# Kernel tuning notes

Measured on AMD Instinct MI355X. Metric: run time of the kernel, lower is better.

The kernel has to match this reference:

```python
import jax, jax.numpy as jnp
import numpy as np

SIZE = 1024      # codebook entries
CODE_DIM = 256   # embedding dim


def setup_inputs() -> dict:
    key = jax.random.key(0)
    k_z, k_w = jax.random.split(key)
    z = jax.random.normal(k_z, (8, CODE_DIM, 16, 32, 32), dtype=jnp.float32)
    # init.uniform_(weight, -1/size, 1/size)
    codebook = jax.random.uniform(
        k_w, (SIZE, CODE_DIM), dtype=jnp.float32,
        minval=-1.0 / SIZE, maxval=1.0 / SIZE)
    return {"z": z, "codebook": codebook}


def reference(z, codebook):
    bs, d, t, h, w = z.shape
    # tokens: [N, d] with N = bs*t*h*w (matches permute(0,2,3,4,1).reshape(-1,d))
    zf = jnp.transpose(z, (0, 2, 3, 4, 1)).reshape(-1, d)
    # squared-distance expansion instead of materializing [size, N, d]:
    # ||z - e||^2 = ||z||^2 - 2 z.e + ||e||^2 ; argmin identical to argmin of norm
    d2 = (jnp.sum(zf * zf, axis=1, keepdims=True)
          - 2.0 * (zf @ codebook.T)
          + jnp.sum(codebook * codebook, axis=1))  # [N, size]
    encoding_indices = jnp.argmin(d2, axis=-1).reshape(bs, t, h, w)
    # gather + permute back to [bs, d, t, h, w]
    quantized = jnp.transpose(codebook[encoding_indices], (0, 4, 1, 2, 3))
    st = z + jax.lax.stop_gradient(quantized - z)  # straight-through output
    return (quantized, st, encoding_indices)
```

## Files before the change

kernel.cpp:

```cpp
#include <hip/hip_runtime.h>
#include <stdint.h>


constexpr int Dd  = 256;
constexpr int SPB = 16384;
constexpr int Nn  = 131072;
constexpr int Kk  = 1024;
constexpr int CCAP = 16;
#define WWIN 2.2e-3f

typedef short short8 __attribute__((ext_vector_type(8)));
typedef float v4f    __attribute__((ext_vector_type(4)));

__device__ __forceinline__ unsigned bf16pk(float a, float b){
  unsigned ua = __float_as_uint(a), ub = __float_as_uint(b);
  ua = (ua + 0x7fffu + ((ua >> 16) & 1u)) >> 16;
  ub = (ub + 0x7fffu + ((ub >> 16) & 1u)) & 0xffff0000u;
  return ua | ub;
}
__device__ __forceinline__ short8 frg(uint4 u){
  union { uint4 a; short8 b; } x; x.a = u; return x.b;
}
__device__ __forceinline__ v4f mfma16(short8 a, short8 b, v4f c){
  return __builtin_amdgcn_mfma_f32_16x16x32_bf16(a, b, c, 0, 0, 0);
}
__device__ __forceinline__ void dma16(const void* g, void* l){
  __builtin_amdgcn_global_load_lds((const __attribute__((address_space(1))) void*)g,
                                   (__attribute__((address_space(3))) void*)l, 16, 0, 0);
}

__global__ __launch_bounds__(64) void cnorm_k(const float* __restrict__ cb,
                                              float* __restrict__ cn){
  const int k = blockIdx.x, l = threadIdx.x;
  const float* row = cb + (size_t)k * Dd;
  float s = 0.f;
  #pragma unroll
  for (int c = 0; c < Dd; c += 64){ float v = row[c + l]; s += v * v; }
  #pragma unroll
  for (int off = 32; off > 0; off >>= 1) s += __shfl_down(s, off, 64);
  if (l == 0) cn[k] = s;
}

__global__ __launch_bounds__(256) void cconv_k(const float* __restrict__ cb,
                                               uint4* __restrict__ Bg){
  const int cc = blockIdx.x, n = threadIdx.x;
  const float* row = cb + (size_t)(cc * 256 + n) * Dd;
  for (int dc = 0; dc < 8; dc++){
    float v[32];
    const float4* rp = (const float4*)(row + dc * 32);
    #pragma unroll
    for (int q = 0; q < 8; q++){
      float4 f = rp[q]; v[4*q]=f.x; v[4*q+1]=f.y; v[4*q+2]=f.z; v[4*q+3]=f.w;
    }
    unsigned hv[16];
    #pragma unroll
    for (int p = 0; p < 16; p++) hv[p] = bf16pk(v[2*p], v[2*p+1]);
    size_t base = ((size_t)cc * 8 + dc) * 1024;
    #pragma unroll
    for (int kq = 0; kq < 4; kq++)
      Bg[base + (size_t)kq*256 + n] = make_uint4(hv[4*kq],hv[4*kq+1],hv[4*kq+2],hv[4*kq+3]);
  }
}

__global__ __launch_bounds__(512, 4) void vq_sweep_k(const float* __restrict__ z,
                                                     const uint4* __restrict__ Bg,
                                                     const float* __restrict__ cnG,
                                                     int* __restrict__ cntW,
                                                     unsigned short* __restrict__ candW,
                                                     int* __restrict__ abestW,
                                                     int* __restrict__ hCntB,
                                                     int* __restrict__ heavyRegion,
                                                     int* __restrict__ idsW,
                                                     float* __restrict__ out){
  __shared__ uint4 Bs[2][2048];
  __shared__ float cnS[1024];
  __shared__ int hN;
  __shared__ int hT[128];

  const int tid = threadIdx.x, bId = blockIdx.x;
  const int w = tid >> 6, ln = tid & 63;
  const int li = ln & 15, lq = ln >> 4;

  if (tid == 0) hN = 0;

  if (w < 4) dma16((const uint4*)cnG + w*64 + ln, (uint4*)&cnS[w*256]);
  int bOff[4];
  #pragma unroll
  for (int j = 0; j < 4; j++){
    const int f = j*512 + tid;
    bOff[j] = (f >> 8)*1024 + ((f >> 6) & 3)*256 + (f & 63);
  }
  #pragma unroll
  for (int j = 0; j < 4; j++)
    dma16(Bg + bOff[j], &Bs[0][j*512 + w*64]);

  const int tok0 = bId * 128;
  const int b = tok0 >> 14;
  const int s0 = tok0 & 16383;
  const float* zb = z + (size_t)b * Dd * SPB + s0;
  short8 aF[8];
  const int tl = w*16 + li;
  #pragma unroll
  for (int kk = 0; kk < 8; kk++){
    float v[8];
    #pragma unroll
    for (int j = 0; j < 8; j++)
      v[j] = zb[(size_t)(kk*32 + lq*8 + j) * SPB + tl];
    union { unsigned u[4]; short8 s8; } x;
    #pragma unroll
    for (int p = 0; p < 4; p++) x.u[p] = bf16pk(v[2*p], v[2*p+1]);
    aF[kk] = x.s8;
  }

  unsigned bestR[4], thrU[4]; int cntR[4];
  #pragma unroll
  for (int i = 0; i < 4; i++){ bestR[i] = 0xFFFFFFFFu; thrU[i] = 0u; cntR[i] = 0; }

  for (int c = 0; c < 16; c++){
    if (c < 15){
      const int cn1 = c + 1;
      const int srcB = (cn1 >> 2)*8192 + (cn1 & 3)*64;
      uint4* dstB = &Bs[cn1 & 1][0];
      #pragma unroll
      for (int j = 0; j < 4; j++)
        dma16(Bg + srcB + bOff[j], dstB + j*512 + w*64);
      asm volatile("s_waitcnt vmcnt(4)" ::: "memory");
    } else {
      asm volatile("s_waitcnt vmcnt(0)" ::: "memory");
    }
    __builtin_amdgcn_s_barrier();
    asm volatile("" ::: "memory");

    v4f acc[4];
    const v4f vz = {0.f, 0.f, 0.f, 0.f};
    #pragma unroll
    for (int ni = 0; ni < 4; ni++) acc[ni] = vz;

    const uint4* Bbase = &Bs[c & 1][lq*64 + li];
    __builtin_amdgcn_s_setprio(1);
    #pragma unroll
    for (int kk = 0; kk < 8; kk++){
      short8 b0 = frg(Bbase[kk*256 +  0]);
      short8 b1 = frg(Bbase[kk*256 + 16]);
      short8 b2 = frg(Bbase[kk*256 + 32]);
      short8 b3 = frg(Bbase[kk*256 + 48]);
      acc[0] = mfma16(aF[kk], b0, acc[0]);
      acc[1] = mfma16(aF[kk], b1, acc[1]);
      acc[2] = mfma16(aF[kk], b2, acc[2]);
      acc[3] = mfma16(aF[kk], b3, acc[3]);
    }
    __builtin_amdgcn_s_setprio(0);

    float cnv[4];
    #pragma unroll
    for (int ni = 0; ni < 4; ni++) cnv[ni] = cnS[c*64 + ni*16 + li];

    const int codeB = c*64 + li;
    #pragma unroll
    for (int r = 0; r < 4; r++){
      unsigned pv[4];
      unsigned pm = 0xFFFFFFFFu;
      #pragma unroll
      for (int ni = 0; ni < 4; ni++){
        float s = fmaf(acc[ni][r], -2.0f, cnv[ni]);
        unsigned u = __float_as_uint(s);
        u ^= (unsigned)((int)u >> 31) | 0x80000000u;
        unsigned p = (u & 0xFFFFFC00u) | (unsigned)(codeB + ni*16);
        pv[ni] = p;
        pm = (pm < p) ? pm : p;
      }
      unsigned pmw = pm;
      #pragma unroll
      for (int off = 1; off < 16; off <<= 1){
        unsigned o = (unsigned)__shfl_xor((int)pmw, off, 16);
        pmw = (pmw < o) ? pmw : o;
      }
      if (pmw <= bestR[r]){
        bestR[r] = pmw;
        unsigned bp = pmw & 0xFFFFFC00u;
        unsigned fb = (bp & 0x80000000u) ? (bp ^ 0x80000000u) : ~bp;
        float thrf = __uint_as_float(fb) + WWIN;
        unsigned tu = __float_as_uint(thrf);
        tu ^= (unsigned)((int)tu >> 31) | 0x80000000u;
        thrU[r] = tu | 1023u;
      }
      if (__any(pm <= thrU[r])){
        const int tok = tok0 + w*16 + lq*4 + r;
        int base = cntR[r];
        #pragma unroll
        for (int ni = 0; ni < 4; ni++){
          const unsigned p = pv[ni];
          const bool pass = (p <= thrU[r]);
          unsigned long long bal = __ballot(pass);
          const unsigned bq = (unsigned)(bal >> (lq*16)) & 0xFFFFu;
          if (pass){
            int pos = base + __popc(bq & ((1u << li) - 1u));
            if (pos < CCAP)
              candW[(size_t)tok*CCAP + pos] = (unsigned short)(p & 1023u);
          }
          base += __popc(bq);
        }
        cntR[r] = base;
      }
    }
    __builtin_amdgcn_s_barrier();
    asm volatile("" ::: "memory");
  }

  if (li == 0){
    #pragma unroll
    for (int r = 0; r < 4; r++){
      const int tok = tok0 + w*16 + lq*4 + r;
      if (cntR[r] == 1){
        const int code = (int)(bestR[r] & 1023u);
        idsW[tok] = code;
        out[(size_t)2 * Nn * Dd + tok] = (float)code;
      } else {
        int p = atomicAdd(&hN, 1);
        hT[p] = tok;
        cntW[tok] = cntR[r];
        abestW[tok] = (int)(bestR[r] & 1023u);
      }
    }
  }
  __syncthreads();
  if (tid == 0) hCntB[bId] = hN;
  if (tid < hN) heavyRegion[bId*128 + tid] = hT[tid];
}

__global__ __launch_bounds__(256) void vq_rescore_k(const float* __restrict__ z,
                                                    const float* __restrict__ cb,
                                                    const float* __restrict__ cnG,
                                                    const int* __restrict__ cntW,
                                                    const unsigned short* __restrict__ candW,
                                                    const int* __restrict__ abestW,
                                                    const int* __restrict__ hCntB,
                                                    const int* __restrict__ heavyRegion,
                                                    int* __restrict__ idsW,
                                                    float* __restrict__ out){
  __shared__ float zS[64][128];
  const int tid = threadIdx.x, reg = blockIdx.x;
  const int h = hCntB[reg];
  if (h == 0) return;

  const int tok0 = reg * 128;
  const int b = tok0 >> 14, sb = tok0 & 16383;
  const float* zb = z + (size_t)b * Dd * SPB + sb;

  const bool act = tid < h;
  int tok = 0, tl = 0, n = 0, abest = 0;
  bool ovf = false;
  unsigned short cds[CCAP];
  if (act){
    tok = heavyRegion[reg*128 + tid];
    tl = tok & 127;
    n = cntW[tok];
    ovf = (n > CCAP);
    if (ovf) n = CCAP;
    *(uint4*)&cds[0] = *(const uint4*)&candW[(size_t)tok * CCAP];
    *(uint4*)&cds[8] = *(const uint4*)&candW[(size_t)tok * CCAP + 8];
    abest = abestW[tok];
  }
  const int eIdx = act ? (ovf ? abest : (int)cds[0]) : 0;

  float accs[CCAP];
  #pragma unroll
  for (int i = 0; i < CCAP; i++) accs[i] = 0.f;
  float accE = 0.f, za = 0.f;

  for (int ch = 0; ch < 4; ch++){
    if (ch) __syncthreads();
    #pragma unroll
    for (int rr = 0; rr < 8; rr++){
      const int f4 = rr*256 + tid;
      const int row = f4 >> 5, c4 = f4 & 31;
      const float4 v = *(const float4*)(zb + (size_t)(ch*64 + row) * SPB + c4*4);
      *(float4*)&zS[row][c4*4] = v;
    }
    __syncthreads();
    if (act){
      #pragma unroll 8
      for (int d = 0; d < 64; d++){
        const float v = zS[d][tl];
        za = fmaf(v, v, za);
      }
      #pragma unroll
      for (int ci = 0; ci < CCAP; ci++){
        if (ci < n){
          const float* cr = cb + (size_t)cds[ci] * Dd + ch*64;
          float a = accs[ci];
          #pragma unroll
          for (int d = 0; d < 64; d += 4){
            const float4 cv = *(const float4*)(cr + d);
            a = fmaf(zS[d+0][tl], cv.x, a);
            a = fmaf(zS[d+1][tl], cv.y, a);
            a = fmaf(zS[d+2][tl], cv.z, a);
            a = fmaf(zS[d+3][tl], cv.w, a);
          }
          accs[ci] = a;
        }
      }
      if (ovf){
        const float* cr = cb + (size_t)eIdx * Dd + ch*64;
        float a = accE;
        #pragma unroll
        for (int d = 0; d < 64; d += 4){
          const float4 cv = *(const float4*)(cr + d);
          a = fmaf(zS[d+0][tl], cv.x, a);
          a = fmaf(zS[d+1][tl], cv.y, a);
          a = fmaf(zS[d+2][tl], cv.z, a);
          a = fmaf(zS[d+3][tl], cv.w, a);
        }
        accE = a;
      }
    }
  }

  if (act){
    float bv = 3.4e38f; int bi = 0x7fffffff;
    #pragma unroll
    for (int ci = 0; ci < CCAP; ci++){
      if (ci < n){
        const int ix = (int)cds[ci];
        float t  = za - 2.0f * accs[ci];
        float d2 = t + cnG[ix];
        if (d2 < bv || (d2 == bv && ix < bi)){ bv = d2; bi = ix; }
      }
    }
    if (ovf){
      float t  = za - 2.0f * accE;
      float d2 = t + cnG[eIdx];
      if (d2 < bv || (d2 == bv && eIdx < bi)){ bv = d2; bi = eIdx; }
    }
    idsW[tok] = bi;
    out[(size_t)2 * Nn * Dd + tok] = (float)bi;
  }
}

__global__ __launch_bounds__(256) void vq_gather_k(const float* __restrict__ cb,
                                                   const int* __restrict__ idsW,
                                                   float* __restrict__ out){
  __shared__ float tile[64][129];
  __shared__ int lid[64];
  const int tid = threadIdx.x, blk = blockIdx.x;
  const int b = blk >> 8, s0 = (blk & 255) * 64;
  if (tid < 64) lid[tid] = idsW[b * SPB + s0 + tid];
  __syncthreads();

  const int r2 = tid >> 7, c = tid & 127;
  const int s = tid & 63, cq = tid >> 6;
  float* qb  = out + (size_t)b * Dd * SPB + s0 + s;
  float* stb = qb + (size_t)Nn * Dd;

  for (int ch = 0; ch < 2; ch++){
    #pragma unroll 4
    for (int t0 = 0; t0 < 64; t0 += 2){
      const int row = t0 + r2;
      tile[row][c] = cb[(size_t)lid[row] * Dd + ch*128 + c];
    }
    __syncthreads();
    #pragma unroll 8
    for (int i = 0; i < 32; i++){
      const int cc2 = i*4 + cq;
      const float v = tile[s][cc2];
      const size_t off = (size_t)(ch*128 + cc2) * SPB;
      qb[off]  = v;
      stb[off] = v;
    }
    __syncthreads();
  }
}

#define MICRO_STEP(WITH_ZN)                                                    \
    {                                                                          \
        float4 a0 = *(const float4*)&As[d][ty * 8];                            \
        float4 a1 = *(const float4*)&As[d][ty * 8 + 4];                        \
        float4 b0 = *(const float4*)&Bs[d][tx * 8];                            \
        float4 b1 = *(const float4*)&Bs[d][tx * 8 + 4];                        \
        float a[8] = {a0.x, a0.y, a0.z, a0.w, a1.x, a1.y, a1.z, a1.w};         \
        float bb[8] = {b0.x, b0.y, b0.z, b0.w, b1.x, b1.y, b1.z, b1.w};        \
        _Pragma("unroll")                                                      \
        for (int i = 0; i < 8; i++) {                                          \
            _Pragma("unroll")                                                  \
            for (int j = 0; j < 8; j++) acc[i][j] += a[i] * bb[j];             \
            if (WITH_ZN) zn[i] += a[i] * a[i];                                 \
        }                                                                      \
    }

__global__ __launch_bounds__(256) void vq_k(const float* __restrict__ z,
                                            const float* __restrict__ cb,
                                            const float* __restrict__ cn,
                                            float* __restrict__ out){
  __shared__ float As[16][128];
  __shared__ float Bs[16][132];
  __shared__ int   idsf[128];
  const int tid = threadIdx.x;
  const int tx = tid & 15, ty = tid >> 4;
  const int blk = blockIdx.x;
  const int b = blk >> 7, sb = (blk & 127) * 128;
  const float* zb = z + (size_t)b * Dd * SPB + sb;
  float bestv[8]; int besti[8]; float zn[8];
  #pragma unroll
  for (int i = 0; i < 8; i++){ bestv[i] = 3.4e38f; besti[i] = 0; zn[i] = 0.f; }
  const int am = tid & 127, ad = tid >> 7;
  const int bd = tid & 15,  bk = tid >> 4;
  for (int cc = 0; cc < 8; cc++){
    float acc[8][8];
    #pragma unroll
    for (int i = 0; i < 8; i++)
      #pragma unroll
      for (int j = 0; j < 8; j++) acc[i][j] = 0.f;
    for (int dc = 0; dc < 16; dc++){
      #pragma unroll
      for (int r = 0; r < 8; r++){
        const int d = ad + r * 2;
        As[d][am] = zb[(size_t)(dc*16 + d) * SPB + am];
      }
      #pragma unroll
      for (int r = 0; r < 8; r++){
        const int k = bk + r * 16;
        Bs[bd][k] = cb[(size_t)(cc*128 + k) * Dd + dc*16 + bd];
      }
      __syncthreads();
      if (cc == 0){
        #pragma unroll
        for (int d = 0; d < 16; d++) MICRO_STEP(1)
      } else {
        #pragma unroll
        for (int d = 0; d < 16; d++) MICRO_STEP(0)
      }
      __syncthreads();
    }
    const float* cnp = cn + cc*128 + tx*8;
    float4 c0 = *(const float4*)cnp;
    float4 c1 = *(const float4*)(cnp + 4);
    float cv[8] = {c0.x, c0.y, c0.z, c0.w, c1.x, c1.y, c1.z, c1.w};
    #pragma unroll
    for (int i = 0; i < 8; i++){
      #pragma unroll
      for (int j = 0; j < 8; j++){
        float t  = zn[i] - 2.0f * acc[i][j];
        float d2 = t + cv[j];
        int   ix = cc*128 + tx*8 + j;
        if (d2 < bestv[i]){ bestv[i] = d2; besti[i] = ix; }
      }
    }
  }
  #pragma unroll
  for (int i = 0; i < 8; i++){
    float v = bestv[i]; int ix = besti[i];
    #pragma unroll
    for (int off = 8; off > 0; off >>= 1){
      float ov = __shfl_down(v, off, 16);
      int   oi = __shfl_down(ix, off, 16);
      if (ov < v || (ov == v && oi < ix)){ v = ov; ix = oi; }
    }
    if (tx == 0) idsf[ty*8 + i] = ix;
  }
  __syncthreads();
  if (tid < 128) out[(size_t)2*Nn*Dd + (size_t)blk*128 + tid] = (float)idsf[tid];
  const int m = tid & 127, cg = tid >> 7;
  const int myidx = idsf[m];
  const float* crow = cb + (size_t)myidx * Dd + cg*128;
  float* q  = out + (size_t)b * Dd * SPB + (size_t)cg * 128 * SPB + sb + m;
  float* st = q + (size_t)Nn * Dd;
  #pragma unroll 8
  for (int r = 0; r < 128; r++){
    const float v = crow[r];
    q[(size_t)r * SPB]  = v;
    st[(size_t)r * SPB] = v;
  }
}

extern "C" void kernel_launch(void* const* d_in, const int* in_sizes, int n_in,
                              void* d_out, int out_size, void* d_ws, size_t ws_size,
                              hipStream_t stream){
  const float* z  = (const float*)d_in[0];
  const float* cb = (const float*)d_in[1];
  float* out = (float*)d_out;

  const size_t BG_B  = (size_t)4 * 8 * 1024 * 16;
  const size_t CN_B  = (size_t)Kk * 4;
  const size_t CNT_B = (size_t)Nn * 4;
  const size_t CAN_B = (size_t)Nn * CCAP * 2;
  const size_t ABW_B = (size_t)Nn * 4;
  const size_t IDS_B = (size_t)Nn * 4;
  const size_t HCB_B = (size_t)(Nn/128) * 4;
  const size_t HR_B  = (size_t)Nn * 4;
  const size_t NEED = BG_B + CN_B + CNT_B + CAN_B + ABW_B + IDS_B + HCB_B + HR_B;

  if (ws_size >= NEED){
    uint8_t* ws = (uint8_t*)d_ws;
    size_t o = 0;
    uint4* Bg   = (uint4*)(ws + o);          o += BG_B;
    float* cnG  = (float*)(ws + o);          o += CN_B;
    int*   cntW = (int*)(ws + o);            o += CNT_B;
    unsigned short* candW = (unsigned short*)(ws + o); o += CAN_B;
    int*   abW  = (int*)(ws + o);            o += ABW_B;
    int*   idsW = (int*)(ws + o);            o += IDS_B;
    int*   hCB  = (int*)(ws + o);            o += HCB_B;
    int*   hReg = (int*)(ws + o);            o += HR_B;

    cnorm_k<<<Kk, 64, 0, stream>>>(cb, cnG);
    cconv_k<<<4, 256, 0, stream>>>(cb, Bg);
    vq_sweep_k<<<Nn/128, 512, 0, stream>>>(z, Bg, cnG, cntW, candW, abW,
                                           hCB, hReg, idsW, out);
    vq_rescore_k<<<Nn/128, 256, 0, stream>>>(z, cb, cnG, cntW, candW, abW,
                                             hCB, hReg, idsW, out);
    vq_gather_k<<<Nn/64, 256, 0, stream>>>(cb, idsW, out);
  } else {
    float* cn = (float*)d_ws;
    cnorm_k<<<Kk, 64, 0, stream>>>(cb, cn);
    vq_k<<<Nn/128, 256, 0, stream>>>(z, cb, cn, out);
  }
}
```

Measured before the change: 606.7 us.

## Software-pipeline sweep epilogue with next MFMA chunk; fuse rescore and gather kernels

The sweep loop is unrolled by two with separate accumulator sets, so the argmin/candidate epilogue of one codebook chunk runs after the MFMAs of the next chunk are issued. This lets the scalar/shuffle epilogue work overlap matrix-core work. Separately, the rescore and gather kernels are merged into one finish kernel that keeps the final indices in shared memory, which removes one launch and the global round trip of the index array. The cost is more accumulator registers in the sweep kernel, which may pressure occupancy under its launch bounds, and fewer, larger blocks for the gather phase.

```diff
diff --git a/kernel.cpp b/kernel.cpp
--- a/kernel.cpp
+++ b/kernel.cpp
@@ -59,6 +59,65 @@
     #pragma unroll
     for (int kq = 0; kq < 4; kq++)
       Bg[base + (size_t)kq*256 + n] = make_uint4(hv[4*kq],hv[4*kq+1],hv[4*kq+2],hv[4*kq+3]);
+  }
+}
+
+__device__ __forceinline__ void epi(const v4f (&acc)[4], const int c,
+                                    const int li, const int lq, const int w,
+                                    const int tok0, const float* cnS,
+                                    unsigned (&bestR)[4], unsigned (&thrU)[4],
+                                    int (&cntR)[4],
+                                    unsigned short* __restrict__ candW){
+  float cnv[4];
+  #pragma unroll
+  for (int ni = 0; ni < 4; ni++) cnv[ni] = cnS[c*64 + ni*16 + li];
+  const int codeB = c*64 + li;
+  #pragma unroll
+  for (int r = 0; r < 4; r++){
+    unsigned pv[4];
+    unsigned pm = 0xFFFFFFFFu;
+    #pragma unroll
+    for (int ni = 0; ni < 4; ni++){
+      float s = fmaf(acc[ni][r], -2.0f, cnv[ni]);
+      unsigned u = __float_as_uint(s);
+      u ^= (unsigned)((int)u >> 31) | 0x80000000u;
+      unsigned p = (u & 0xFFFFFC00u) | (unsigned)(codeB + ni*16);
+      pv[ni] = p;
+      pm = (pm < p) ? pm : p;
+    }
+    unsigned pmw = pm;
+    #pragma unroll
+    for (int off = 1; off < 16; off <<= 1){
+      unsigned o = (unsigned)__shfl_xor((int)pmw, off, 16);
+      pmw = (pmw < o) ? pmw : o;
+    }
+    if (pmw <= bestR[r]){
+      bestR[r] = pmw;
+      unsigned bp = pmw & 0xFFFFFC00u;
+      unsigned fb = (bp & 0x80000000u) ? (bp ^ 0x80000000u) : ~bp;
+      float thrf = __uint_as_float(fb) + WWIN;
+      unsigned tu = __float_as_uint(thrf);
+      tu ^= (unsigned)((int)tu >> 31) | 0x80000000u;
+      thrU[r] = tu | 1023u;
+    }
+    if (__any(pm <= thrU[r])){
+      const int tok = tok0 + w*16 + lq*4 + r;
+      int base = cntR[r];
+      #pragma unroll
+      for (int ni = 0; ni < 4; ni++){
+        const unsigned p = pv[ni];
+        const bool pass = (p <= thrU[r]);
+        unsigned long long bal = __ballot(pass);
+        const unsigned bq = (unsigned)(bal >> (lq*16)) & 0xFFFFu;
+        if (pass){
+          int pos = base + __popc(bq & ((1u << li) - 1u));
+          if (pos < CCAP)
+            candW[(size_t)tok*CCAP + pos] = (unsigned short)(p & 1023u);
+        }
+        base += __popc(bq);
+      }
+      cntR[r] = base;
+    }
   }
 }
 
@@ -116,96 +175,80 @@
   #pragma unroll
   for (int i = 0; i < 4; i++){ bestR[i] = 0xFFFFFFFFu; thrU[i] = 0u; cntR[i] = 0; }
 
-  for (int c = 0; c < 16; c++){
-    if (c < 15){
-      const int cn1 = c + 1;
+  v4f accA[4], accB[4];
+  const v4f vz = {0.f, 0.f, 0.f, 0.f};
+
+  for (int cp = 0; cp < 8; cp++){
+    const int c0 = cp*2, c1 = c0 + 1;
+
+    {
+      const int cn1 = c0 + 1;
       const int srcB = (cn1 >> 2)*8192 + (cn1 & 3)*64;
-      uint4* dstB = &Bs[cn1 & 1][0];
       #pragma unroll
       for (int j = 0; j < 4; j++)
-        dma16(Bg + srcB + bOff[j], dstB + j*512 + w*64);
+        dma16(Bg + srcB + bOff[j], &Bs[1][j*512 + w*64]);
       asm volatile("s_waitcnt vmcnt(4)" ::: "memory");
-    } else {
-      asm volatile("s_waitcnt vmcnt(0)" ::: "memory");
-    }
-    __builtin_amdgcn_s_barrier();
-    asm volatile("" ::: "memory");
-
-    v4f acc[4];
-    const v4f vz = {0.f, 0.f, 0.f, 0.f};
-    #pragma unroll
-    for (int ni = 0; ni < 4; ni++) acc[ni] = vz;
-
-    const uint4* Bbase = &Bs[c & 1][lq*64 + li];
-    __builtin_amdgcn_s_setprio(1);
-    #pragma unroll
-    for (int kk = 0; kk < 8; kk++){
-      short8 b0 = frg(Bbase[kk*256 +  0]);
-      short8 b1 = frg(Bbase[kk*256 + 16]);
-      short8 b2 = frg(Bbase[kk*256 + 32]);
-      short8 b3 = frg(Bbase[kk*256 + 48]);
-      acc[0] = mfma16(aF[kk], b0, acc[0]);
-      acc[1] = mfma16(aF[kk], b1, acc[1]);
-      acc[2] = mfma16(aF[kk], b2, acc[2]);
-      acc[3] = mfma16(aF[kk], b3, acc[3]);
-    }
-    __builtin_amdgcn_s_setprio(0);
-
-    float cnv[4];
-    #pragma unroll
-    for (int ni = 0; ni < 4; ni++) cnv[ni] = cnS[c*64 + ni*16 + li];
-
-    const int codeB = c*64 + li;
-    #pragma unroll
-    for (int r = 0; r < 4; r++){
-      unsigned pv[4];
-      unsigned pm = 0xFFFFFFFFu;
-      #pragma unroll
-      for (int ni = 0; ni < 4; ni++){
-        float s = fmaf(acc[ni][r], -2.0f, cnv[ni]);
-        unsigned u = __float_as_uint(s);
-        u ^= (unsigned)((int)u >> 31) | 0x80000000u;
-        unsigned p = (u & 0xFFFFFC00u) | (unsigned)(codeB + ni*16);
-        pv[ni] = p;
-        pm = (pm < p) ? pm : p;
-      }
-      unsigned pmw = pm;
-      #pragma unroll
-      for (int off = 1; off < 16; off <<= 1){
-        unsigned o = (unsigned)__shfl_xor((int)pmw, off, 16);
-        pmw = (pmw < o) ? pmw : o;
-      }
-      if (pmw <= bestR[r]){
-        bestR[r] = pmw;
-        unsigned bp = pmw & 0xFFFFFC00u;
-        unsigned fb = (bp & 0x80000000u) ? (bp ^ 0x80000000u) : ~bp;
-        float thrf = __uint_as_float(fb) + WWIN;
-        unsigned tu = __float_as_uint(thrf);
-        tu ^= (unsigned)((int)tu >> 31) | 0x80000000u;
-        thrU[r] = tu | 1023u;
-      }
-      if (__any(pm <= thrU[r])){
-        const int tok = tok0 + w*16 + lq*4 + r;
-        int base = cntR[r];
+      __builtin_amdgcn_s_barrier();
+      asm volatile("" ::: "memory");
+
+      #pragma unroll
+      for (int ni = 0; ni < 4; ni++) accA[ni] = vz;
+      const uint4* Bbase = &Bs[0][lq*64 + li];
+      __builtin_amdgcn_s_setprio(1);
+      #pragma unroll
+      for (int kk = 0; kk < 8; kk++){
+        short8 b0 = frg(Bbase[kk*256 +  0]);
+        short8 b1 = frg(Bbase[kk*256 + 16]);
+        short8 b2 = frg(Bbase[kk*256 + 32]);
+        short8 b3 = frg(Bbase[kk*256 + 48]);
+        accA[0] = mfma16(aF[kk], b0, accA[0]);
+        accA[1] = mfma16(aF[kk], b1, accA[1]);
+        accA[2] = mfma16(aF[kk], b2, accA[2]);
+        accA[3] = mfma16(aF[kk], b3, accA[3]);
+      }
+      __builtin_amdgcn_s_setprio(0);
+      if (cp)
+        epi(accB, c0 - 1, li, lq, w, tok0, cnS, bestR, thrU, cntR, candW);
+      __builtin_amdgcn_s_barrier();
+      asm volatile("" ::: "memory");
+    }
+
+    {
+      if (c1 < 15){
+        const int cn1 = c1 + 1;
+        const int srcB = (cn1 >> 2)*8192 + (cn1 & 3)*64;
         #pragma unroll
-        for (int ni = 0; ni < 4; ni++){
-          const unsigned p = pv[ni];
-          const bool pass = (p <= thrU[r]);
-          unsigned long long bal = __ballot(pass);
-          const unsigned bq = (unsigned)(bal >> (lq*16)) & 0xFFFFu;
-          if (pass){
-            int pos = base + __popc(bq & ((1u << li) - 1u));
-            if (pos < CCAP)
-              candW[(size_t)tok*CCAP + pos] = (unsigned short)(p & 1023u);
-          }
-          base += __popc(bq);
-        }
-        cntR[r] = base;
-      }
-    }
-    __builtin_amdgcn_s_barrier();
-    asm volatile("" ::: "memory");
-  }
+        for (int j = 0; j < 4; j++)
+          dma16(Bg + srcB + bOff[j], &Bs[0][j*512 + w*64]);
+        asm volatile("s_waitcnt vmcnt(4)" ::: "memory");
+      } else {
+        asm volatile("s_waitcnt vmcnt(0)" ::: "memory");
+      }
+      __builtin_amdgcn_s_barrier();
+      asm volatile("" ::: "memory");
+
+      #pragma unroll
+      for (int ni = 0; ni < 4; ni++) accB[ni] = vz;
+      const uint4* Bbase = &Bs[1][lq*64 + li];
+      __builtin_amdgcn_s_setprio(1);
+      #pragma unroll
+      for (int kk = 0; kk < 8; kk++){
+        short8 b0 = frg(Bbase[kk*256 +  0]);
+        short8 b1 = frg(Bbase[kk*256 + 16]);
+        short8 b2 = frg(Bbase[kk*256 + 32]);
+        short8 b3 = frg(Bbase[kk*256 + 48]);
+        accB[0] = mfma16(aF[kk], b0, accB[0]);
+        accB[1] = mfma16(aF[kk], b1, accB[1]);
+        accB[2] = mfma16(aF[kk], b2, accB[2]);
+        accB[3] = mfma16(aF[kk], b3, accB[3]);
+      }
+      __builtin_amdgcn_s_setprio(0);
+      epi(accA, c0, li, lq, w, tok0, cnS, bestR, thrU, cntR, candW);
+      __builtin_amdgcn_s_barrier();
+      asm volatile("" ::: "memory");
+    }
+  }
+  epi(accB, 15, li, lq, w, tok0, cnS, bestR, thrU, cntR, candW);
 
   if (li == 0){
     #pragma unroll
@@ -228,146 +271,145 @@
   if (tid < hN) heavyRegion[bId*128 + tid] = hT[tid];
 }
 
-__global__ __launch_bounds__(256) void vq_rescore_k(const float* __restrict__ z,
-                                                    const float* __restrict__ cb,
-                                                    const float* __restrict__ cnG,
-                                                    const int* __restrict__ cntW,
-                                                    const unsigned short* __restrict__ candW,
-                                                    const int* __restrict__ abestW,
-                                                    const int* __restrict__ hCntB,
-                                                    const int* __restrict__ heavyRegion,
-                                                    int* __restrict__ idsW,
-                                                    float* __restrict__ out){
-  __shared__ float zS[64][128];
+__global__ __launch_bounds__(256) void vq_finish_k(const float* __restrict__ z,
+                                                   const float* __restrict__ cb,
+                                                   const float* __restrict__ cnG,
+                                                   const int* __restrict__ cntW,
+                                                   const unsigned short* __restrict__ candW,
+                                                   const int* __restrict__ abestW,
+                                                   const int* __restrict__ hCntB,
+                                                   const int* __restrict__ heavyRegion,
+                                                   const int* __restrict__ idsW,
+                                                   float* __restrict__ out){
+  __shared__ __align__(16) float smem[64*129];
+  __shared__ int idS[128];
+
   const int tid = threadIdx.x, reg = blockIdx.x;
-  const int h = hCntB[reg];
-  if (h == 0) return;
-
   const int tok0 = reg * 128;
   const int b = tok0 >> 14, sb = tok0 & 16383;
-  const float* zb = z + (size_t)b * Dd * SPB + sb;
-
-  const bool act = tid < h;
-  int tok = 0, tl = 0, n = 0, abest = 0;
-  bool ovf = false;
-  unsigned short cds[CCAP];
-  if (act){
-    tok = heavyRegion[reg*128 + tid];
-    tl = tok & 127;
-    n = cntW[tok];
-    ovf = (n > CCAP);
-    if (ovf) n = CCAP;
-    *(uint4*)&cds[0] = *(const uint4*)&candW[(size_t)tok * CCAP];
-    *(uint4*)&cds[8] = *(const uint4*)&candW[(size_t)tok * CCAP + 8];
-    abest = abestW[tok];
-  }
-  const int eIdx = act ? (ovf ? abest : (int)cds[0]) : 0;
-
-  float accs[CCAP];
-  #pragma unroll
-  for (int i = 0; i < CCAP; i++) accs[i] = 0.f;
-  float accE = 0.f, za = 0.f;
-
-  for (int ch = 0; ch < 4; ch++){
-    if (ch) __syncthreads();
-    #pragma unroll
-    for (int rr = 0; rr < 8; rr++){
-      const int f4 = rr*256 + tid;
-      const int row = f4 >> 5, c4 = f4 & 31;
-      const float4 v = *(const float4*)(zb + (size_t)(ch*64 + row) * SPB + c4*4);
-      *(float4*)&zS[row][c4*4] = v;
-    }
-    __syncthreads();
+
+  if (tid < 128) idS[tid] = idsW[tok0 + tid];
+
+  const int h = hCntB[reg];
+  if (h > 0){
+    float* zS = smem;
+    const float* zb = z + (size_t)b * Dd * SPB + sb;
+
+    const bool act = tid < h;
+    int tok = 0, tl = 0, n = 0, abest = 0;
+    bool ovf = false;
+    unsigned short cds[CCAP];
     if (act){
-      #pragma unroll 8
-      for (int d = 0; d < 64; d++){
-        const float v = zS[d][tl];
-        za = fmaf(v, v, za);
-      }
-      #pragma unroll
-      for (int ci = 0; ci < CCAP; ci++){
-        if (ci < n){
-          const float* cr = cb + (size_t)cds[ci] * Dd + ch*64;
-          float a = accs[ci];
+      tok = heavyRegion[reg*128 + tid];
+      tl = tok & 127;
+      n = cntW[tok];
+      ovf = (n > CCAP);
+      if (ovf) n = CCAP;
+      *(uint4*)&cds[0] = *(const uint4*)&candW[(size_t)tok * CCAP];
+      *(uint4*)&cds[8] = *(const uint4*)&candW[(size_t)tok * CCAP + 8];
+      abest = abestW[tok];
+    }
+    const int eIdx = act ? (ovf ? abest : (int)cds[0]) : 0;
+
+    float accs[CCAP];
+    #pragma unroll
+    for (int i = 0; i < CCAP; i++) accs[i] = 0.f;
+    float accE = 0.f, za = 0.f;
+
+    for (int ch = 0; ch < 4; ch++){
+      if (ch) __syncthreads();
+      #pragma unroll
+      for (int rr = 0; rr < 8; rr++){
+        const int f4 = rr*256 + tid;
+        const int row = f4 >> 5, c4 = f4 & 31;
+        const float4 v = *(const float4*)(zb + (size_t)(ch*64 + row) * SPB + c4*4);
+        *(float4*)&zS[row*128 + c4*4] = v;
+      }
+      __syncthreads();
+      if (act){
+        #pragma unroll 8
+        for (int d = 0; d < 64; d++){
+          const float v = zS[d*128 + tl];
+          za = fmaf(v, v, za);
+        }
+        #pragma unroll
+        for (int ci = 0; ci < CCAP; ci++){
+          if (ci < n){
+            const float* cr = cb + (size_t)cds[ci] * Dd + ch*64;
+            float a = accs[ci];
+            #pragma unroll
+            for (int d = 0; d < 64; d += 4){
+              const float4 cv = *(const float4*)(cr + d);
+              a = fmaf(zS[(d+0)*128 + tl], cv.x, a);
+              a = fmaf(zS[(d+1)*128 + tl], cv.y, a);
+              a = fmaf(zS[(d+2)*128 + tl], cv.z, a);
+              a = fmaf(zS[(d+3)*128 + tl], cv.w, a);
+            }
+            accs[ci] = a;
+          }
+        }
+        if (ovf){
+          const float* cr = cb + (size_t)eIdx * Dd + ch*64;
+          float a = accE;
           #pragma unroll
           for (int d = 0; d < 64; d += 4){
             const float4 cv = *(const float4*)(cr + d);
-            a = fmaf(zS[d+0][tl], cv.x, a);
-            a = fmaf(zS[d+1][tl], cv.y, a);
-            a = fmaf(zS[d+2][tl], cv.z, a);
-            a = fmaf(zS[d+3][tl], cv.w, a);
+            a = fmaf(zS[(d+0)*128 + tl], cv.x, a);
+            a = fmaf(zS[(d+1)*128 + tl], cv.y, a);
+            a = fmaf(zS[(d+2)*128 + tl], cv.z, a);
+            a = fmaf(zS[(d+3)*128 + tl], cv.w, a);
           }
-          accs[ci] = a;
+          accE = a;
         }
       }
+    }
+
+    if (act){
+      float bv = 3.4e38f; int bi = 0x7fffffff;
+      #pragma unroll
+      for (int ci = 0; ci < CCAP; ci++){
+        if (ci < n){
+          const int ix = (int)cds[ci];
+          float t  = za - 2.0f * accs[ci];
+          float d2 = t + cnG[ix];
+          if (d2 < bv || (d2 == bv && ix < bi)){ bv = d2; bi = ix; }
+        }
+      }
       if (ovf){
-        const float* cr = cb + (size_t)eIdx * Dd + ch*64;
-        float a = accE;
-        #pragma unroll
-        for (int d = 0; d < 64; d += 4){
-          const float4 cv = *(const float4*)(cr + d);
-          a = fmaf(zS[d+0][tl], cv.x, a);
-          a = fmaf(zS[d+1][tl], cv.y, a);
-          a = fmaf(zS[d+2][tl], cv.z, a);
-          a = fmaf(zS[d+3][tl], cv.w, a);
-        }
-        accE = a;
-      }
-    }
-  }
-
-  if (act){
-    float bv = 3.4e38f; int bi = 0x7fffffff;
-    #pragma unroll
-    for (int ci = 0; ci < CCAP; ci++){
-      if (ci < n){
-        const int ix = (int)cds[ci];
-        float t  = za - 2.0f * accs[ci];
-        float d2 = t + cnG[ix];
-        if (d2 < bv || (d2 == bv && ix < bi)){ bv = d2; bi = ix; }
-      }
-    }
-    if (ovf){
-      float t  = za - 2.0f * accE;
-      float d2 = t + cnG[eIdx];
-      if (d2 < bv || (d2 == bv && eIdx < bi)){ bv = d2; bi = eIdx; }
-    }
-    idsW[tok] = bi;
-    out[(size_t)2 * Nn * Dd + tok] = (float)bi;
-  }
-}
-
-__global__ __launch_bounds__(256) void vq_gather_k(const float* __restrict__ cb,
-                                                   const int* __restrict__ idsW,
-                                                   float* __restrict__ out){
-  __shared__ float tile[64][129];
-  __shared__ int lid[64];
-  const int tid = threadIdx.x, blk = blockIdx.x;
-  const int b = blk >> 8, s0 = (blk & 255) * 64;
-  if (tid < 64) lid[tid] = idsW[b * SPB + s0 + tid];
+        float t  = za - 2.0f * accE;
+        float d2 = t + cnG[eIdx];
+        if (d2 < bv || (d2 == bv && eIdx < bi)){ bv = d2; bi = eIdx; }
+      }
+      idS[tl] = bi;
+      out[(size_t)2 * Nn * Dd + tok] = (float)bi;
+    }
+  }
   __syncthreads();
 
-  const int r2 = tid >> 7, c = tid & 127;
+  float* tile = smem;
+  const int r2 = tid >> 7, ccol = tid & 127;
   const int s = tid & 63, cq = tid >> 6;
-  float* qb  = out + (size_t)b * Dd * SPB + s0 + s;
-  float* stb = qb + (size_t)Nn * Dd;
-
-  for (int ch = 0; ch < 2; ch++){
-    #pragma unroll 4
-    for (int t0 = 0; t0 < 64; t0 += 2){
-      const int row = t0 + r2;
-      tile[row][c] = cb[(size_t)lid[row] * Dd + ch*128 + c];
-    }
-    __syncthreads();
-    #pragma unroll 8
-    for (int i = 0; i < 32; i++){
-      const int cc2 = i*4 + cq;
-      const float v = tile[s][cc2];
-      const size_t off = (size_t)(ch*128 + cc2) * SPB;
-      qb[off]  = v;
-      stb[off] = v;
-    }
-    __syncthreads();
+  for (int hh = 0; hh < 2; hh++){
+    const int s0h = hh * 64;
+    float* qb  = out + (size_t)b * Dd * SPB + sb + s0h + s;
+    float* stb = qb + (size_t)Nn * Dd;
+    for (int ch = 0; ch < 2; ch++){
+      if (hh | ch) __syncthreads();
+      #pragma unroll 4
+      for (int t0 = 0; t0 < 64; t0 += 2){
+        const int row = t0 + r2;
+        tile[row*129 + ccol] = cb[(size_t)idS[s0h + row] * Dd + ch*128 + ccol];
+      }
+      __syncthreads();
+      #pragma unroll 8
+      for (int i = 0; i < 32; i++){
+        const int cc2 = i*4 + cq;
+        const float v = tile[s*129 + cc2];
+        const size_t off = (size_t)(ch*128 + cc2) * SPB;
+        qb[off]  = v;
+        stb[off] = v;
+      }
+    }
   }
 }
 
@@ -505,9 +547,8 @@
     cconv_k<<<4, 256, 0, stream>>>(cb, Bg);
     vq_sweep_k<<<Nn/128, 512, 0, stream>>>(z, Bg, cnG, cntW, candW, abW,
                                            hCB, hReg, idsW, out);
-    vq_rescore_k<<<Nn/128, 256, 0, stream>>>(z, cb, cnG, cntW, candW, abW,
-                                             hCB, hReg, idsW, out);
-    vq_gather_k<<<Nn/64, 256, 0, stream>>>(cb, idsW, out);
+    vq_finish_k<<<Nn/128, 256, 0, stream>>>(z, cb, cnG, cntW, candW, abW,
+                                            hCB, hReg, idsW, out);
   } else {
     float* cn = (float*)d_ws;
     cnorm_k<<<Kk, 64, 0, stream>>>(cb, cn);
```

After: 597.8 us. About the same (-1.5%).
